# Performance work log

Hardware: AMD Instinct MI355X
Metric: run time of the kernel (lower is better)

The kernel has to match this reference:

```python
import jax, jax.numpy as jnp
import numpy as np

N = 4096      # total children nodes
NSEL = 1024   # selected nodes per forward (len(idIndexes))
D = 32        # singleDim (box is [lower|upper], each D dims)
K = 128       # omega embedding dim
EPS = 1e-05   # clip_by_min default
PI_HALF = float(np.pi / 2)
W_DIST = 1.0
W_OVL = 1.0
W_EXC = 1.0
W_SHP = 1.0


def setup_inputs() -> dict:
    key = jax.random.key(0)
    ks = jax.random.split(key, 6)
    # learned box params: lower/upper corners, upper = lower + positive width
    childrenLower = jax.random.uniform(ks[0], (N, D), dtype=jnp.float32)
    childrenHigher = childrenLower + 0.1 * jax.random.uniform(ks[1], (N, D), dtype=jnp.float32)
    # parent box shifted by circleRange (correspondingParentsEmbL_/H_ in torch)
    parentL_ = jnp.full((D,), 0.0, dtype=jnp.float32)
    parentH_ = jnp.full((D,), 2.0, dtype=jnp.float32)
    parentRange = jnp.maximum(parentH_ - parentL_, EPS)  # clip_by_min(H-L)
    # leaves-count ratio per child (positive, sums to 1)
    leavesRatio = jax.nn.softmax(jax.random.normal(ks[2], (N,), dtype=jnp.float32))
    idIndexes = jax.random.randint(ks[3], (NSEL,), 0, N)
    omegaEmb = jax.random.normal(ks[4], (NSEL, K), dtype=jnp.float32)
    return {
        "childrenLower": childrenLower,
        "childrenHigher": childrenHigher,
        "parentL_": parentL_,
        "parentH_": parentH_,
        "parentRange": parentRange,
        "leavesRatio": leavesRatio,
        "omegaEmb": omegaEmb,
        "idIndexes": idIndexes,
        "epoch": 0,
    }


def _hierarchy_loss(childrenLower, childrenHigher, parentL_, parentH_,
                    parentRange, leavesRatio, omegaEmb, idIndexes):
    L = childrenLower[idIndexes]   # [n, d] selected lower corners
    H = childrenHigher[idIndexes]  # [n, d]
    n = L.shape[0]

    # ---- exceed loss: children boxes must stay inside parent box ----
    lossExceed = (jax.nn.relu(parentL_ - L).sum()
                  + jax.nn.relu(H - parentH_).sum()
                  + jax.nn.relu(parentL_ - H).sum()
                  + jax.nn.relu(L - parentH_).sum())

    diff = H - L  # [n, d] box widths

    # ---- overlap loss: per-dim pairwise box intersection length ----
    Lt = L.T  # [d, n]
    Ht = H.T  # [d, n]
    maxLower = jnp.maximum(Lt[:, :, None], Lt[:, None, :])   # [d, n, n]
    minHigher = jnp.minimum(Ht[:, :, None], Ht[:, None, :])  # [d, n, n]
    offdiag = 1.0 - jnp.eye(n, dtype=L.dtype)                # mask self-pairs
    lossOverlap = jax.nn.relu((minHigher - maxLower) * offdiag).sum()

    # ---- shape loss: width ratio should match leaves-count ratio ----
    num = jnp.maximum(diff / parentRange, EPS)               # clip_by_min
    den = leavesRatio[idIndexes][:, None]                    # [n, 1]
    sdiv = jnp.clip(num / den, 0.01, 1.99)                   # clip_by_max(ma=1.99, mi=0.01)
    lossShape = jnp.abs(jnp.tan((sdiv - 1.0) * PI_HALF)).sum()

    # ---- distance loss: pairwise center dist vs omega-embedding dist ----
    mid = 0.5 * (L + H)                                       # [n, d] box centers
    midT = mid.T                                              # [d, n]
    d2 = jnp.square(jnp.abs(midT[:, :, None] - midT[:, None, :])).sum(0)  # [n, n]
    dN = d2 / jnp.maximum(jnp.linalg.norm(d2), EPS)
    ip = jnp.sum(omegaEmb * omegaEmb, axis=1, keepdims=True)  # [n, 1]
    oD = jnp.maximum(-2.0 * (omegaEmb @ omegaEmb.T) + ip + ip.T, EPS)
    oN = oD / jnp.maximum(jnp.linalg.norm(oD), EPS)
    lossDistance = jnp.linalg.norm(dN - oN)

    return (W_DIST * lossDistance + W_OVL * lossOverlap
            + W_EXC * lossExceed + W_SHP * lossShape)


def reference(childrenLower, childrenHigher, parentL_, parentH_,
              parentRange, leavesRatio, omegaEmb, idIndexes, epoch):
    # epoch % 2 == 0 branch of the original forward (distance+overlap+exceed+shape)
    return _hierarchy_loss(childrenLower, childrenHigher, parentL_, parentH_,
                           parentRange, leavesRatio, omegaEmb, idIndexes)
```

## Files before the change

kernel.cpp:

```cpp
#include <hip/hip_runtime.h>
#include <math.h>

#define NSELC 1024
#define DDIM  32
#define KDIM  128
#define TILE  64
#define LDSP  68
#define EPSF  1e-5f
#define PIH   1.57079632679489662f
#define NBLK  256

__device__ __forceinline__ float waveReduce(float v) {
    #pragma unroll
    for (int o = 32; o > 0; o >>= 1) v += __shfl_down(v, o, 64);
    return v;
}

__global__ __launch_bounds__(256) void pair_kernel(
    const float* __restrict__ CL, const float* __restrict__ CH,
    const float* __restrict__ PL, const float* __restrict__ PH,
    const float* __restrict__ PR, const float* __restrict__ LR,
    const float* __restrict__ OM, const int* __restrict__ IDX,
    float* __restrict__ PART)
{
    const int t  = threadIdx.x;
    const int tx = t & 15, ty = t >> 4;
    const int bi = blockIdx.x >> 4, bj = blockIdx.x & 15;
    const int iBase = bi * TILE, jBase = bj * TILE;

    __shared__ float sm[4 * DDIM * LDSP];
    __shared__ int   sIdxI[TILE];
    __shared__ float sred[5 * 4];

    float* sLI = sm;
    float* sHI = sm + DDIM * LDSP;
    float* sLJ = sm + 2 * DDIM * LDSP;
    float* sHJ = sm + 3 * DDIM * LDSP;
    float* sOI = sm;
    float* sOJ = sm + 2 * DDIM * LDSP;

    {
        const int row  = t & 63;
        const int buf  = t >> 6;
        const int base = (buf < 2) ? iBase : jBase;
        const int gidx = IDX[base + row];
        if (buf == 0) sIdxI[row] = gidx;
        const float* src = ((buf & 1) ? CH : CL) + gidx * DDIM;
        float* dst = sm + buf * DDIM * LDSP;
        #pragma unroll
        for (int c8 = 0; c8 < 8; ++c8) {
            float4 v = *(const float4*)(src + 4 * c8);
            dst[(4*c8+0) * LDSP + row] = v.x;
            dst[(4*c8+1) * LDSP + row] = v.y;
            dst[(4*c8+2) * LDSP + row] = v.z;
            dst[(4*c8+3) * LDSP + row] = v.w;
        }
    }
    __syncthreads();

    float d2[16];
    #pragma unroll
    for (int p = 0; p < 16; ++p) d2[p] = 0.f;
    float ovl = 0.f;
    const bool diagT = (bi == bj) && (tx == ty);

    for (int d = 0; d < DDIM; ++d) {
        const float4 li = *(const float4*)&sLI[d * LDSP + 4 * ty];
        const float4 hi = *(const float4*)&sHI[d * LDSP + 4 * ty];
        const float4 lj = *(const float4*)&sLJ[d * LDSP + 4 * tx];
        const float4 hj = *(const float4*)&sHJ[d * LDSP + 4 * tx];
        float liA[4] = {li.x, li.y, li.z, li.w};
        float hiA[4] = {hi.x, hi.y, hi.z, hi.w};
        float ljA[4] = {lj.x, lj.y, lj.z, lj.w};
        float hjA[4] = {hj.x, hj.y, hj.z, hj.w};
        float miA[4], mjA[4];
        #pragma unroll
        for (int r = 0; r < 4; ++r) {
            miA[r] = 0.5f * (liA[r] + hiA[r]);
            mjA[r] = 0.5f * (ljA[r] + hjA[r]);
        }
        #pragma unroll
        for (int r = 0; r < 4; ++r) {
            #pragma unroll
            for (int c = 0; c < 4; ++c) {
                float dm = miA[r] - mjA[c];
                d2[r*4+c] = fmaf(dm, dm, d2[r*4+c]);
                float ov = fminf(hiA[r], hjA[c]) - fmaxf(liA[r], ljA[c]);
                ovl += fmaxf(ov, 0.f);
            }
        }
        if (diagT) {
            #pragma unroll
            for (int r = 0; r < 4; ++r) ovl -= fmaxf(hiA[r] - liA[r], 0.f);
        }
    }

    float es = 0.f;
    if (bj == 0) {
        const int row = t & 63;
        const int d0  = (t >> 6) * 8;
        const float den = LR[sIdxI[row]];
        #pragma unroll
        for (int k = 0; k < 8; ++k) {
            const int d = d0 + k;
            float l  = sLI[d * LDSP + row], h = sHI[d * LDSP + row];
            float pl = PL[d], ph = PH[d], pr = PR[d];
            es += fmaxf(pl - l, 0.f) + fmaxf(h - ph, 0.f)
                + fmaxf(pl - h, 0.f) + fmaxf(l - ph, 0.f);
            float num  = fmaxf((h - l) / pr, EPSF);
            float sdiv = fminf(fmaxf(num / den, 0.01f), 1.99f);
            es += fabsf(tanf((sdiv - 1.0f) * PIH));
        }
    }

    float ssd[16];
    #pragma unroll
    for (int p = 0; p < 16; ++p) ssd[p] = 0.f;

    const float4* OM4 = (const float4*)OM;
    for (int kc = 0; kc < 2; ++kc) {
        __syncthreads();
        {
            const int row  = t & 63;
            const int obuf = (t >> 6) & 1;
            const int half = t >> 7;
            const int base = obuf ? jBase : iBase;
            float* dst = obuf ? sOJ : sOI;
            #pragma unroll
            for (int c8 = 0; c8 < 8; ++c8) {
                const int kk = half * 32 + c8 * 4;
                float4 v = OM4[(base + row) * (KDIM/4) + (kc * TILE + kk) / 4];
                dst[(kk+0) * LDSP + row] = v.x;
                dst[(kk+1) * LDSP + row] = v.y;
                dst[(kk+2) * LDSP + row] = v.z;
                dst[(kk+3) * LDSP + row] = v.w;
            }
        }
        __syncthreads();
        for (int k = 0; k < TILE; ++k) {
            const float4 oi = *(const float4*)&sOI[k * LDSP + 4 * ty];
            const float4 oj = *(const float4*)&sOJ[k * LDSP + 4 * tx];
            float oiA[4] = {oi.x, oi.y, oi.z, oi.w};
            float ojA[4] = {oj.x, oj.y, oj.z, oj.w};
            #pragma unroll
            for (int r = 0; r < 4; ++r) {
                #pragma unroll
                for (int c = 0; c < 4; ++c) {
                    float dm = oiA[r] - ojA[c];
                    ssd[r*4+c] = fmaf(dm, dm, ssd[r*4+c]);
                }
            }
        }
    }

    float sdd = 0.f, soo = 0.f, sdo = 0.f;
    #pragma unroll
    for (int p = 0; p < 16; ++p) {
        float a = d2[p];
        float b = fmaxf(ssd[p], EPSF);
        sdd = fmaf(a, a, sdd);
        soo = fmaf(b, b, soo);
        sdo = fmaf(a, b, sdo);
    }

    float vals[5] = {sdd, soo, sdo, ovl, es};
    const int wave = t >> 6, lane = t & 63;
    #pragma unroll
    for (int q = 0; q < 5; ++q) {
        float r = waveReduce(vals[q]);
        if (lane == 0) sred[q * 4 + wave] = r;
    }
    __syncthreads();
    if (t < 5) {
        float s = sred[t*4+0] + sred[t*4+1] + sred[t*4+2] + sred[t*4+3];
        PART[blockIdx.x * 5 + t] = s;
    }
}

__global__ __launch_bounds__(256) void fin_kernel(const float* __restrict__ PART,
                                                  float* __restrict__ OUT) {
    const int t = threadIdx.x;
    float v[5];
    #pragma unroll
    for (int q = 0; q < 5; ++q) v[q] = PART[t * 5 + q];

    __shared__ float sred[5 * 4];
    const int wave = t >> 6, lane = t & 63;
    #pragma unroll
    for (int q = 0; q < 5; ++q) {
        float r = waveReduce(v[q]);
        if (lane == 0) sred[q * 4 + wave] = r;
    }
    __syncthreads();
    if (t == 0) {
        float a[5];
        #pragma unroll
        for (int q = 0; q < 5; ++q)
            a[q] = sred[q*4+0] + sred[q*4+1] + sred[q*4+2] + sred[q*4+3];
        float Sdd = a[0], Soo = a[1], Sdo = a[2], Sovl = a[3], Ses = a[4];
        float Nd = fmaxf(sqrtf(Sdd), EPSF);
        float No = fmaxf(sqrtf(Soo), EPSF);
        float w  = Sdd / (Nd * Nd) - 2.f * Sdo / (Nd * No) + Soo / (No * No);
        OUT[0] = sqrtf(fmaxf(w, 0.f)) + Sovl + Ses;
    }
}

extern "C" void kernel_launch(void* const* d_in, const int* in_sizes, int n_in,
                              void* d_out, int out_size, void* d_ws, size_t ws_size,
                              hipStream_t stream) {
    const float* CL  = (const float*)d_in[0];
    const float* CH  = (const float*)d_in[1];
    const float* PL  = (const float*)d_in[2];
    const float* PH  = (const float*)d_in[3];
    const float* PR  = (const float*)d_in[4];
    const float* LR  = (const float*)d_in[5];
    const float* OM  = (const float*)d_in[6];
    const int*   IDX = (const int*)d_in[7];

    float* PART = (float*)d_ws;
    pair_kernel<<<dim3(NBLK), dim3(256), 0, stream>>>(CL, CH, PL, PH, PR, LR, OM, IDX, PART);
    fin_kernel<<<dim3(1), dim3(256), 0, stream>>>(PART, (float*)d_out);
}
```

Baseline: 92.16 us.

## Compute pairwise distances via bf16 MFMA Gram matrices with norm expansion

Replaces the scalar pairwise squared-difference loops for the omega-embedding and box-center distances with the expansion |a|^2+|b|^2-2a·b. The dot products are computed with bf16 16x16x32 MFMA instructions, and the row norms are computed in fp32 during tile loading. This removes most of the VALU FMA work and the two-pass omega staging with its extra barriers. In exchange, inputs are rounded to bf16 and the subtraction form can cancel catastrophically for near points, so accuracy of the distance loss may degrade.

Measured after the change: 86.23 us. 6.4% less time.

```diff
diff --git a/kernel.cpp b/kernel.cpp
--- a/kernel.cpp
+++ b/kernel.cpp
@@ -5,15 +5,25 @@
 #define DDIM  32
 #define KDIM  128
 #define TILE  64
-#define LDSP  68
+#define BOXP  68
+#define OMP   136
+#define MIDP  40
 #define EPSF  1e-5f
 #define PIH   1.57079632679489662f
 #define NBLK  256
 
+typedef short s16x8 __attribute__((ext_vector_type(8)));
+typedef float f32x4 __attribute__((ext_vector_type(4)));
+
 __device__ __forceinline__ float waveReduce(float v) {
     #pragma unroll
     for (int o = 32; o > 0; o >>= 1) v += __shfl_down(v, o, 64);
     return v;
+}
+
+__device__ __forceinline__ short bf16c(float x) {
+    unsigned u = __float_as_uint(x);
+    return (short)((u + 0x8000u) >> 16);
 }
 
 __global__ __launch_bounds__(256) void pair_kernel(
@@ -23,68 +33,97 @@
     const float* __restrict__ OM, const int* __restrict__ IDX,
     float* __restrict__ PART)
 {
-    const int t  = threadIdx.x;
+    const int t    = threadIdx.x;
+    const int lane = t & 63, wave = t >> 6;
     const int tx = t & 15, ty = t >> 4;
     const int bi = blockIdx.x >> 4, bj = blockIdx.x & 15;
     const int iBase = bi * TILE, jBase = bj * TILE;
 
-    __shared__ float sm[4 * DDIM * LDSP];
+    __shared__ float sBox[4 * DDIM * BOXP];
+    __shared__ short sOm [2 * TILE * OMP] __attribute__((aligned(16)));
+    __shared__ short sMid[2 * TILE * MIDP] __attribute__((aligned(16)));
+    __shared__ float sNm[2 * TILE];
+    __shared__ float sNw[2 * TILE];
     __shared__ int   sIdxI[TILE];
     __shared__ float sred[5 * 4];
 
-    float* sLI = sm;
-    float* sHI = sm + DDIM * LDSP;
-    float* sLJ = sm + 2 * DDIM * LDSP;
-    float* sHJ = sm + 3 * DDIM * LDSP;
-    float* sOI = sm;
-    float* sOJ = sm + 2 * DDIM * LDSP;
-
-    {
+    float* sLI = sBox;
+    float* sHI = sBox + DDIM * BOXP;
+    float* sLJ = sBox + 2 * DDIM * BOXP;
+    float* sHJ = sBox + 3 * DDIM * BOXP;
+
+    if (t < 128) {
+        const int tile = t >> 6;
         const int row  = t & 63;
-        const int buf  = t >> 6;
-        const int base = (buf < 2) ? iBase : jBase;
+        const int base = tile ? jBase : iBase;
         const int gidx = IDX[base + row];
-        if (buf == 0) sIdxI[row] = gidx;
-        const float* src = ((buf & 1) ? CH : CL) + gidx * DDIM;
-        float* dst = sm + buf * DDIM * LDSP;
-        #pragma unroll
-        for (int c8 = 0; c8 < 8; ++c8) {
-            float4 v = *(const float4*)(src + 4 * c8);
-            dst[(4*c8+0) * LDSP + row] = v.x;
-            dst[(4*c8+1) * LDSP + row] = v.y;
-            dst[(4*c8+2) * LDSP + row] = v.z;
-            dst[(4*c8+3) * LDSP + row] = v.w;
-        }
+        if (tile == 0) sIdxI[row] = gidx;
+        const float4* L4 = (const float4*)CL + gidx * (DDIM / 4);
+        const float4* H4 = (const float4*)CH + gidx * (DDIM / 4);
+        float* dL = sBox + 2 * tile * DDIM * BOXP;
+        float* dH = dL + DDIM * BOXP;
+        float mids[DDIM];
+        float nm = 0.f;
+        #pragma unroll
+        for (int c = 0; c < 8; ++c) {
+            float4 l = L4[c], h = H4[c];
+            dL[(4*c+0) * BOXP + row] = l.x;  dH[(4*c+0) * BOXP + row] = h.x;
+            dL[(4*c+1) * BOXP + row] = l.y;  dH[(4*c+1) * BOXP + row] = h.y;
+            dL[(4*c+2) * BOXP + row] = l.z;  dH[(4*c+2) * BOXP + row] = h.z;
+            dL[(4*c+3) * BOXP + row] = l.w;  dH[(4*c+3) * BOXP + row] = h.w;
+            float mx = 0.5f * (l.x + h.x), my = 0.5f * (l.y + h.y);
+            float mz = 0.5f * (l.z + h.z), mw = 0.5f * (l.w + h.w);
+            mids[4*c+0] = mx; mids[4*c+1] = my; mids[4*c+2] = mz; mids[4*c+3] = mw;
+            nm = fmaf(mx, mx, nm); nm = fmaf(my, my, nm);
+            nm = fmaf(mz, mz, nm); nm = fmaf(mw, mw, nm);
+        }
+        sNm[tile * TILE + row] = nm;
+        short* dM = sMid + tile * TILE * MIDP + row * MIDP;
+        #pragma unroll
+        for (int c8 = 0; c8 < 4; ++c8) {
+            s16x8 s;
+            #pragma unroll
+            for (int j = 0; j < 8; ++j) s[j] = bf16c(mids[c8 * 8 + j]);
+            *(s16x8*)(dM + c8 * 8) = s;
+        }
+    } else {
+        const int u    = t - 128;
+        const int tile = u >> 6;
+        const int row  = u & 63;
+        const int base = tile ? jBase : iBase;
+        const float4* O4 = (const float4*)OM + (base + row) * (KDIM / 4);
+        short* dO = sOm + tile * TILE * OMP + row * OMP;
+        float nw = 0.f;
+        #pragma unroll
+        for (int c8 = 0; c8 < 16; ++c8) {
+            float4 a = O4[2 * c8], b = O4[2 * c8 + 1];
+            nw = fmaf(a.x, a.x, nw); nw = fmaf(a.y, a.y, nw);
+            nw = fmaf(a.z, a.z, nw); nw = fmaf(a.w, a.w, nw);
+            nw = fmaf(b.x, b.x, nw); nw = fmaf(b.y, b.y, nw);
+            nw = fmaf(b.z, b.z, nw); nw = fmaf(b.w, b.w, nw);
+            s16x8 s = { bf16c(a.x), bf16c(a.y), bf16c(a.z), bf16c(a.w),
+                        bf16c(b.x), bf16c(b.y), bf16c(b.z), bf16c(b.w) };
+            *(s16x8*)(dO + c8 * 8) = s;
+        }
+        sNw[tile * TILE + row] = nw;
     }
     __syncthreads();
 
-    float d2[16];
-    #pragma unroll
-    for (int p = 0; p < 16; ++p) d2[p] = 0.f;
     float ovl = 0.f;
     const bool diagT = (bi == bj) && (tx == ty);
-
     for (int d = 0; d < DDIM; ++d) {
-        const float4 li = *(const float4*)&sLI[d * LDSP + 4 * ty];
-        const float4 hi = *(const float4*)&sHI[d * LDSP + 4 * ty];
-        const float4 lj = *(const float4*)&sLJ[d * LDSP + 4 * tx];
-        const float4 hj = *(const float4*)&sHJ[d * LDSP + 4 * tx];
+        const float4 li = *(const float4*)&sLI[d * BOXP + 4 * ty];
+        const float4 hi = *(const float4*)&sHI[d * BOXP + 4 * ty];
+        const float4 lj = *(const float4*)&sLJ[d * BOXP + 4 * tx];
+        const float4 hj = *(const float4*)&sHJ[d * BOXP + 4 * tx];
         float liA[4] = {li.x, li.y, li.z, li.w};
         float hiA[4] = {hi.x, hi.y, hi.z, hi.w};
         float ljA[4] = {lj.x, lj.y, lj.z, lj.w};
         float hjA[4] = {hj.x, hj.y, hj.z, hj.w};
-        float miA[4], mjA[4];
-        #pragma unroll
-        for (int r = 0; r < 4; ++r) {
-            miA[r] = 0.5f * (liA[r] + hiA[r]);
-            mjA[r] = 0.5f * (ljA[r] + hjA[r]);
-        }
         #pragma unroll
         for (int r = 0; r < 4; ++r) {
             #pragma unroll
             for (int c = 0; c < 4; ++c) {
-                float dm = miA[r] - mjA[c];
-                d2[r*4+c] = fmaf(dm, dm, d2[r*4+c]);
                 float ov = fminf(hiA[r], hjA[c]) - fmaxf(liA[r], ljA[c]);
                 ovl += fmaxf(ov, 0.f);
             }
@@ -97,13 +136,13 @@
 
     float es = 0.f;
     if (bj == 0) {
-        const int row = t & 63;
-        const int d0  = (t >> 6) * 8;
+        const int row = lane;
+        const int d0  = wave * 8;
         const float den = LR[sIdxI[row]];
         #pragma unroll
         for (int k = 0; k < 8; ++k) {
             const int d = d0 + k;
-            float l  = sLI[d * LDSP + row], h = sHI[d * LDSP + row];
+            float l  = sLI[d * BOXP + row], h = sHI[d * BOXP + row];
             float pl = PL[d], ph = PH[d], pr = PR[d];
             es += fmaxf(pl - l, 0.f) + fmaxf(h - ph, 0.f)
                 + fmaxf(pl - h, 0.f) + fmaxf(l - ph, 0.f);
@@ -113,58 +152,55 @@
         }
     }
 
-    float ssd[16];
-    #pragma unroll
-    for (int p = 0; p < 16; ++p) ssd[p] = 0.f;
-
-    const float4* OM4 = (const float4*)OM;
-    for (int kc = 0; kc < 2; ++kc) {
-        __syncthreads();
-        {
-            const int row  = t & 63;
-            const int obuf = (t >> 6) & 1;
-            const int half = t >> 7;
-            const int base = obuf ? jBase : iBase;
-            float* dst = obuf ? sOJ : sOI;
-            #pragma unroll
-            for (int c8 = 0; c8 < 8; ++c8) {
-                const int kk = half * 32 + c8 * 4;
-                float4 v = OM4[(base + row) * (KDIM/4) + (kc * TILE + kk) / 4];
-                dst[(kk+0) * LDSP + row] = v.x;
-                dst[(kk+1) * LDSP + row] = v.y;
-                dst[(kk+2) * LDSP + row] = v.z;
-                dst[(kk+3) * LDSP + row] = v.w;
-            }
-        }
-        __syncthreads();
-        for (int k = 0; k < TILE; ++k) {
-            const float4 oi = *(const float4*)&sOI[k * LDSP + 4 * ty];
-            const float4 oj = *(const float4*)&sOJ[k * LDSP + 4 * tx];
-            float oiA[4] = {oi.x, oi.y, oi.z, oi.w};
-            float ojA[4] = {oj.x, oj.y, oj.z, oj.w};
-            #pragma unroll
-            for (int r = 0; r < 4; ++r) {
-                #pragma unroll
-                for (int c = 0; c < 4; ++c) {
-                    float dm = oiA[r] - ojA[c];
-                    ssd[r*4+c] = fmaf(dm, dm, ssd[r*4+c]);
-                }
-            }
+    const int m    = lane & 15;
+    const int quad = lane >> 4;
+    const short* oI = sOm;
+    const short* oJ = sOm + TILE * OMP;
+    const short* mI = sMid;
+    const short* mJ = sMid + TILE * MIDP;
+
+    f32x4 accO[4], accM[4];
+    #pragma unroll
+    for (int ct = 0; ct < 4; ++ct) {
+        accO[ct] = (f32x4){0.f, 0.f, 0.f, 0.f};
+        accM[ct] = (f32x4){0.f, 0.f, 0.f, 0.f};
+    }
+    #pragma unroll
+    for (int kc = 0; kc < 4; ++kc) {
+        s16x8 a = *(const s16x8*)&oI[(wave * 16 + m) * OMP + kc * 32 + quad * 8];
+        #pragma unroll
+        for (int ct = 0; ct < 4; ++ct) {
+            s16x8 b = *(const s16x8*)&oJ[(ct * 16 + m) * OMP + kc * 32 + quad * 8];
+            accO[ct] = __builtin_amdgcn_mfma_f32_16x16x32_bf16(a, b, accO[ct], 0, 0, 0);
+        }
+    }
+    {
+        s16x8 a = *(const s16x8*)&mI[(wave * 16 + m) * MIDP + quad * 8];
+        #pragma unroll
+        for (int ct = 0; ct < 4; ++ct) {
+            s16x8 b = *(const s16x8*)&mJ[(ct * 16 + m) * MIDP + quad * 8];
+            accM[ct] = __builtin_amdgcn_mfma_f32_16x16x32_bf16(a, b, accM[ct], 0, 0, 0);
         }
     }
 
     float sdd = 0.f, soo = 0.f, sdo = 0.f;
     #pragma unroll
-    for (int p = 0; p < 16; ++p) {
-        float a = d2[p];
-        float b = fmaxf(ssd[p], EPSF);
-        sdd = fmaf(a, a, sdd);
-        soo = fmaf(b, b, soo);
-        sdo = fmaf(a, b, sdo);
+    for (int ct = 0; ct < 4; ++ct) {
+        const int jL = ct * 16 + m;
+        const float nmJv = sNm[TILE + jL];
+        const float nwJv = sNw[TILE + jL];
+        #pragma unroll
+        for (int r = 0; r < 4; ++r) {
+            const int iL = wave * 16 + quad * 4 + r;
+            float d2v = fmaxf(sNm[iL] + nmJv - 2.f * accM[ct][r], 0.f);
+            float bv  = fmaxf(sNw[iL] + nwJv - 2.f * accO[ct][r], EPSF);
+            sdd = fmaf(d2v, d2v, sdd);
+            soo = fmaf(bv,  bv,  soo);
+            sdo = fmaf(d2v, bv,  sdo);
+        }
     }
 
     float vals[5] = {sdd, soo, sdo, ovl, es};
-    const int wave = t >> 6, lane = t & 63;
     #pragma unroll
     for (int q = 0; q < 5; ++q) {
         float r = waveReduce(vals[q]);
```
